# Kernel optimization log

Measured on AMD Instinct MI355X. Metric: run time of the kernel, lower is better.

Reference implementation:

```python
import jax, jax.numpy as jnp
import numpy as np

EPS = 1e-6


def _make_coord_3d(D, H, W, dtype):
    # torch make_coord_3d(flatten=False).permute(3,0,1,2): channels stacked as (x, y, z)
    lz = jnp.linspace(-1.0, 1.0, D, dtype=dtype)
    ly = jnp.linspace(-1.0, 1.0, H, dtype=dtype)
    lx = jnp.linspace(-1.0, 1.0, W, dtype=dtype)
    cz, cy, cx = jnp.meshgrid(lz, ly, lx, indexing='ij')
    return jnp.stack([cx, cy, cz], axis=0)  # [3, D, H, W]


def _trilinear_border(vol, gd, gh, gw):
    # vol: [C, D, H, W]; gd/gh/gw: [Q] normalized coords for the D/H/W axes.
    # Matches torch grid_sample(mode='bilinear', align_corners=False, padding_mode='border').
    C, D, H, W = vol.shape
    z = (gd + 1.0) * (D * 0.5) - 0.5
    y = (gh + 1.0) * (H * 0.5) - 0.5
    x = (gw + 1.0) * (W * 0.5) - 0.5
    z0 = jnp.floor(z); y0 = jnp.floor(y); x0 = jnp.floor(x)
    wz = (z - z0)[None]; wy = (y - y0)[None]; wx = (x - x0)[None]  # [1, Q]
    z0i = jnp.clip(z0.astype(jnp.int32), 0, D - 1); z1i = jnp.clip(z0.astype(jnp.int32) + 1, 0, D - 1)
    y0i = jnp.clip(y0.astype(jnp.int32), 0, H - 1); y1i = jnp.clip(y0.astype(jnp.int32) + 1, 0, H - 1)
    x0i = jnp.clip(x0.astype(jnp.int32), 0, W - 1); x1i = jnp.clip(x0.astype(jnp.int32) + 1, 0, W - 1)
    g = lambda zi, yi, xi: vol[:, zi, yi, xi]  # gather -> [C, Q]
    return (g(z0i, y0i, x0i) * (1 - wz) * (1 - wy) * (1 - wx)
            + g(z0i, y0i, x1i) * (1 - wz) * (1 - wy) * wx
            + g(z0i, y1i, x0i) * (1 - wz) * wy * (1 - wx)
            + g(z0i, y1i, x1i) * (1 - wz) * wy * wx
            + g(z1i, y0i, x0i) * wz * (1 - wy) * (1 - wx)
            + g(z1i, y0i, x1i) * wz * (1 - wy) * wx
            + g(z1i, y1i, x0i) * wz * wy * (1 - wx)
            + g(z1i, y1i, x1i) * wz * wy * wx)


def _forward(inp, coord, cell, W0, b0, W1, b1, W2, b2, W3, b3):
    feat = inp  # identity encoder: inp is the latent feature grid
    B, C, D, H, W = feat.shape
    rx = 2.0 / D / 2.0; ry = 2.0 / H / 2.0; rz = 2.0 / W / 2.0
    sizes = jnp.array([D, H, W], dtype=feat.dtype)
    feat_coord = _make_coord_3d(D, H, W, feat.dtype)  # [3, D, H, W]
    sample_b = jax.vmap(_trilinear_border, in_axes=(0, 0, 0, 0))
    sample_c = jax.vmap(_trilinear_border, in_axes=(None, 0, 0, 0))

    rel_cell = cell * sizes  # [B, Q, 3]
    cell_vol = jnp.abs(cell[..., 0] * cell[..., 1] * cell[..., 2])
    scale_sq = jnp.clip(8.0 / (cell_vol + 1e-8), 1.0, 64.0)[..., None]  # [B, Q, 1]

    def mlp(x):
        h = jax.nn.relu(x @ W0 + b0)
        h = jax.nn.relu(h @ W1 + b1)
        h = jax.nn.relu(h @ W2 + b2)
        return h @ W3 + b3

    preds, areas = [], []
    for vx in (-1, 1):
        for vy in (-1, 1):
            for vz in (-1, 1):
                shift = jnp.array([vx * rx + EPS, vy * ry + EPS, vz * rz + EPS], dtype=coord.dtype)
                c = jnp.clip(coord + shift, -1.0 + 1e-6, 1.0 - 1e-6)
                gd, gh, gw = c[..., 0], c[..., 1], c[..., 2]
                q_feat = sample_b(feat, gd, gh, gw).transpose(0, 2, 1)        # [B, Q, C]
                q_coord = sample_c(feat_coord, gd, gh, gw).transpose(0, 2, 1)  # [B, Q, 3]
                rel_coord = (coord - q_coord) * sizes
                x = jnp.concatenate([q_feat, rel_coord, rel_cell, scale_sq], axis=-1)
                preds.append(mlp(x))  # [B, Q, 1]
                areas.append(jnp.abs(rel_coord[..., 0] * rel_coord[..., 1] * rel_coord[..., 2]) + 1e-9)
    tot_area = jnp.stack(areas).sum(axis=0)
    areas = areas[::-1]  # local-ensemble diagonal-swap of areas
    ret = sum(p * (a / tot_area)[..., None] for p, a in zip(preds, areas))
    return ret


def setup_inputs() -> dict:
    key = jax.random.key(0)
    ks = jax.random.split(key, 8)
    B, C, D, Q, HID = 1, 64, 32, 131072, 256
    in_dim = C + 3 + 3 + 1  # 71
    w = lambda k, shape, fan_in: jax.random.normal(k, shape, jnp.float32) * (1.0 / np.sqrt(fan_in))
    inp = jax.random.normal(ks[0], (B, C, D, D, D), jnp.float32)
    coord = jax.random.uniform(ks[1], (B, Q, 3), jnp.float32, -1.0, 1.0)
    cell = jnp.full((B, Q, 3), 2.0 / 64.0, jnp.float32)  # uniform cell size of a 64^3 query grid
    return {
        'inp': inp, 'coord': coord, 'cell': cell,
        'W0': w(ks[2], (in_dim, HID), in_dim), 'b0': jnp.zeros((HID,), jnp.float32),
        'W1': w(ks[3], (HID, HID), HID), 'b1': jnp.zeros((HID,), jnp.float32),
        'W2': w(ks[4], (HID, HID), HID), 'b2': jnp.zeros((HID,), jnp.float32),
        'W3': w(ks[5], (HID, 1), HID), 'b3': jnp.zeros((1,), jnp.float32),
    }


def reference(inp, coord, cell, W0, b0, W1, b1, W2, b2, W3, b3):
    return _forward(inp, coord, cell, W0, b0, W1, b1, W2, b2, W3, b3)
```

## Files before the change

kernel.cpp:

```cpp
#include <hip/hip_runtime.h>

typedef __attribute__((ext_vector_type(8))) short s16x8;
typedef __attribute__((ext_vector_type(4))) float f32x4;

__device__ __forceinline__ unsigned short f2bf(float x) {
  unsigned u = __float_as_uint(x);
  u = (u + 0x7fffu + ((u >> 16) & 1u)) >> 16;
  return (unsigned short)u;
}
__device__ __forceinline__ unsigned cvt_pk_bf16(float a, float b) {
  unsigned r;
  asm("v_cvt_pk_bf16_f32 %0, %1, %2" : "=v"(r) : "v"(a), "v"(b));
  return r;
}
__device__ __forceinline__ float bflo(unsigned v) { return __uint_as_float(v << 16); }
__device__ __forceinline__ float bfhi(unsigned v) { return __uint_as_float(v & 0xffff0000u); }

__device__ __forceinline__ void lgkm_barrier() {
  asm volatile("s_waitcnt lgkmcnt(0)" ::: "memory");
  __builtin_amdgcn_s_barrier();
  asm volatile("" ::: "memory");
}

#define FEAT_OFF 0
#define W0F_OFF  2097152
#define W1F_OFF  (W0F_OFF + 24576)
#define W2F_OFF  (W1F_OFF + 65536)
#define W3P_OFF  (W2F_OFF + 65536)
#define WS_TOTAL (W3P_OFF + 512)

__device__ __forceinline__ int col_log(int kp) {
  return (kp & 0xC0) | ((kp & 3) << 4) | ((kp >> 2) & 15);
}

__global__ void liif_prep(const float* __restrict__ inp,
                          const float* __restrict__ W0,
                          const float* __restrict__ W1,
                          const float* __restrict__ W2,
                          const float* __restrict__ W3,
                          unsigned short* __restrict__ ws) {
  int tid = blockIdx.x * 256 + threadIdx.x;
  if (tid < 2097152) {
    int pos = tid >> 6, c = tid & 63;
    ws[FEAT_OFF + tid] = f2bf(inp[c * 32768 + pos]);
  } else if (tid < W1F_OFF) {
    int e = tid - W0F_OFF;
    int j = e & 7, L = (e >> 3) & 63, nt = (e >> 9) & 15, c = e >> 13;
    int k = c * 32 + (L >> 4) * 8 + j, n = nt * 16 + (L & 15);
    ws[tid] = (k < 71) ? f2bf(W0[k * 256 + n]) : (unsigned short)0;
  } else if (tid < W2F_OFF) {
    int e = tid - W1F_OFF;
    int j = e & 7, L = (e >> 3) & 63, nt = (e >> 9) & 15, c = e >> 13;
    int kp = c * 32 + (L >> 4) * 8 + j, n = nt * 16 + (L & 15);
    ws[tid] = f2bf(W1[col_log(kp) * 256 + n]);
  } else if (tid < W3P_OFF) {
    int e = tid - W2F_OFF;
    int j = e & 7, L = (e >> 3) & 63, nt = (e >> 9) & 15, c = e >> 13;
    int kp = c * 32 + (L >> 4) * 8 + j, n = nt * 16 + (L & 15);
    ws[tid] = f2bf(W2[col_log(kp) * 256 + n]);
  } else if (tid < W3P_OFF + 256) {
    int e = tid - W3P_OFF;
    float* w3p = (float*)(ws + W3P_OFF);
    w3p[e] = W3[col_log(e)];
  }
}

template<int KC, bool PRE>
__device__ __forceinline__ void run_layer(const unsigned short* __restrict__ Wf,
                                          const float* __restrict__ bias,
                                          const unsigned short* A, int astride,
                                          unsigned short* H,
                                          const unsigned short* __restrict__ Wnext,
                                          s16x8 (&nb)[4],
                                          int wave, int quad, int l16, int lane) {
  f32x4 acc[4][4];
#pragma unroll
  for (int ntl = 0; ntl < 4; ++ntl) {
    float bv = bias[(wave * 4 + ntl) * 16 + l16];
    f32x4 ai = (f32x4){bv, bv, bv, bv};
#pragma unroll
    for (int rt = 0; rt < 4; ++rt) acc[rt][ntl] = ai;
  }

  __builtin_amdgcn_s_setprio(1);
#pragma unroll
  for (int c = 0; c < KC; ++c) {
    s16x8 a[4];
#pragma unroll
    for (int rt = 0; rt < 4; ++rt)
      a[rt] = *(const s16x8*)(A + (rt * 16 + l16) * astride + c * 32 + quad * 8);
#pragma unroll
    for (int ntl = 0; ntl < 4; ++ntl) {
      int nt = wave * 4 + ntl;
      s16x8 b = (c == 0) ? nb[ntl]
                         : *(const s16x8*)(Wf + (((c * 16 + nt) * 64 + lane) << 3));
#pragma unroll
      for (int rt = 0; rt < 4; ++rt)
        acc[rt][ntl] = __builtin_amdgcn_mfma_f32_16x16x32_bf16(a[rt], b, acc[rt][ntl], 0, 0, 0);
    }
  }
  __builtin_amdgcn_s_setprio(0);

  if constexpr (PRE) {
#pragma unroll
    for (int ntl = 0; ntl < 4; ++ntl)
      nb[ntl] = *(const s16x8*)(Wnext + (((wave * 4 + ntl) * 64 + lane) << 3));
  }

  lgkm_barrier();

  const int cbase = wave * 64 + l16 * 4;
#pragma unroll
  for (int rt = 0; rt < 4; ++rt) {
#pragma unroll
    for (int i = 0; i < 4; ++i) {
      float v0 = fmaxf(acc[rt][0][i], 0.0f);
      float v1 = fmaxf(acc[rt][1][i], 0.0f);
      float v2 = fmaxf(acc[rt][2][i], 0.0f);
      float v3 = fmaxf(acc[rt][3][i], 0.0f);
      int r = rt * 16 + quad * 4 + i;
      uint2 pw = make_uint2(cvt_pk_bf16(v0, v1), cvt_pk_bf16(v2, v3));
      *(uint2*)(H + r * 264 + cbase) = pw;
    }
  }
  lgkm_barrier();
}

__global__ __launch_bounds__(256, 4)
void liif_main(const float* __restrict__ coord,
               const float* __restrict__ cell,
               const float* __restrict__ b0,
               const float* __restrict__ b1,
               const float* __restrict__ b2,
               const float* __restrict__ b3,
               const unsigned short* __restrict__ ws,
               float* __restrict__ out) {
  __shared__ __align__(16) unsigned short sm_h[64 * 264];
  __shared__ float sm_area[64];
  __shared__ float sm_pred[64];
  unsigned short* sm_x = sm_h;

  const unsigned short* feat = ws + FEAT_OFF;
  const int tid = threadIdx.x;
  const int lane = tid & 63;
  const int wave = tid >> 6;
  const int quad = lane >> 4;
  const int l16 = lane & 15;

  s16x8 nb[4];
#pragma unroll
  for (int ntl = 0; ntl < 4; ++ntl)
    nb[ntl] = *(const s16x8*)(ws + W0F_OFF + (((wave * 4 + ntl) * 64 + lane) << 3));

  {
    const int row = tid >> 2, p = tid & 3;
    const int ql = row >> 3, s = row & 7;
    const int q = blockIdx.x * 8 + ql;
    const float c0r = coord[q * 3 + 0], c1r = coord[q * 3 + 1], c2r = coord[q * 3 + 2];
    const float R = 0.03125f;
    const float sh0 = ((s & 4) ? R : -R) + 1e-6f;
    const float sh1 = ((s & 2) ? R : -R) + 1e-6f;
    const float sh2 = ((s & 1) ? R : -R) + 1e-6f;
    const float LO = -1.0f + 1e-6f, HI = 1.0f - 1e-6f;
    float c0 = fminf(fmaxf(c0r + sh0, LO), HI);
    float c1 = fminf(fmaxf(c1r + sh1, LO), HI);
    float c2 = fminf(fmaxf(c2r + sh2, LO), HI);
    float z = (c0 + 1.0f) * 16.0f - 0.5f;
    float y = (c1 + 1.0f) * 16.0f - 0.5f;
    float x = (c2 + 1.0f) * 16.0f - 0.5f;
    float zf = floorf(z), yf = floorf(y), xf = floorf(x);
    float wz = z - zf, wy = y - yf, wx = x - xf;
    int z0 = min(max((int)zf, 0), 31), z1 = min(max((int)zf + 1, 0), 31);
    int y0 = min(max((int)yf, 0), 31), y1 = min(max((int)yf + 1, 0), 31);
    int x0 = min(max((int)xf, 0), 31), x1 = min(max((int)xf + 1, 0), 31);
    float wz0 = 1.0f - wz, wy0 = 1.0f - wy, wx0 = 1.0f - wx;

    float w[8] = { wz0 * wy0 * wx0, wz0 * wy0 * wx, wz0 * wy * wx0, wz0 * wy * wx,
                   wz  * wy0 * wx0, wz  * wy0 * wx, wz  * wy * wx0, wz  * wy * wx };
    int idx[8] = { (z0 * 32 + y0) * 32 + x0, (z0 * 32 + y0) * 32 + x1,
                   (z0 * 32 + y1) * 32 + x0, (z0 * 32 + y1) * 32 + x1,
                   (z1 * 32 + y0) * 32 + x0, (z1 * 32 + y0) * 32 + x1,
                   (z1 * 32 + y1) * 32 + x0, (z1 * 32 + y1) * 32 + x1 };

    float acc[16];
#pragma unroll
    for (int i = 0; i < 16; ++i) acc[i] = 0.0f;
#pragma unroll
    for (int corner = 0; corner < 8; ++corner) {
      const uint4* cp = (const uint4*)(feat + idx[corner] * 64 + p * 16);
      uint4 v0 = cp[0], v1 = cp[1];
      float wc = w[corner];
      unsigned vv[8] = { v0.x, v0.y, v0.z, v0.w, v1.x, v1.y, v1.z, v1.w };
#pragma unroll
      for (int d = 0; d < 8; ++d) {
        acc[2 * d]     += wc * bflo(vv[d]);
        acc[2 * d + 1] += wc * bfhi(vv[d]);
      }
    }
    unsigned pw[8];
#pragma unroll
    for (int d = 0; d < 8; ++d)
      pw[d] = cvt_pk_bf16(acc[2 * d], acc[2 * d + 1]);
    uint4* dst = (uint4*)(&sm_x[row * 104 + p * 16]);
    dst[0] = make_uint4(pw[0], pw[1], pw[2], pw[3]);
    dst[1] = make_uint4(pw[4], pw[5], pw[6], pw[7]);

    if (p == 0) {
      const float step = 2.0f / 31.0f;
      float qc0 = wx0 * (-1.0f + step * x0) + wx * (-1.0f + step * x1);
      float qc1 = wy0 * (-1.0f + step * y0) + wy * (-1.0f + step * y1);
      float qc2 = wz0 * (-1.0f + step * z0) + wz * (-1.0f + step * z1);
      float rel0 = (c0r - qc0) * 32.0f;
      float rel1 = (c1r - qc1) * 32.0f;
      float rel2 = (c2r - qc2) * 32.0f;
      sm_area[row] = fabsf(rel0 * rel1 * rel2) + 1e-9f;
      float cl0 = cell[q * 3 + 0], cl1 = cell[q * 3 + 1], cl2 = cell[q * 3 + 2];
      float ssq = fminf(fmaxf(8.0f / (fabsf(cl0 * cl1 * cl2) + 1e-8f), 1.0f), 64.0f);
      unsigned tw0 = cvt_pk_bf16(rel0, rel1);
      unsigned tw1 = cvt_pk_bf16(rel2, cl0 * 32.0f);
      unsigned tw2 = cvt_pk_bf16(cl1 * 32.0f, cl2 * 32.0f);
      unsigned tw3 = cvt_pk_bf16(ssq, 0.0f);
      uint4* d2 = (uint4*)(&sm_x[row * 104 + 64]);
      d2[0] = make_uint4(tw0, tw1, tw2, tw3);
      d2[1] = make_uint4(0, 0, 0, 0);
      d2[2] = make_uint4(0, 0, 0, 0);
      d2[3] = make_uint4(0, 0, 0, 0);
    }
  }
  lgkm_barrier();

  run_layer<3, true >(ws + W0F_OFF, b0, sm_x, 104, sm_h, ws + W1F_OFF, nb, wave, quad, l16, lane);
  run_layer<8, true >(ws + W1F_OFF, b1, sm_h, 264, sm_h, ws + W2F_OFF, nb, wave, quad, l16, lane);
  run_layer<8, false>(ws + W2F_OFF, b2, sm_h, 264, sm_h, nullptr,      nb, wave, quad, l16, lane);

  {
    const int row = tid >> 2, p = tid & 3;
    const unsigned short* hp = sm_h + row * 264 + p * 64;
    const float* W3p = (const float*)(ws + W3P_OFF);
    float sum = 0.0f;
#pragma unroll
    for (int kk = 0; kk < 8; ++kk) {
      const uint4 v = *(const uint4*)(hp + kk * 8);
      const float4 wa = *(const float4*)(W3p + p * 64 + kk * 8);
      const float4 wb = *(const float4*)(W3p + p * 64 + kk * 8 + 4);
      sum += wa.x * bflo(v.x) + wa.y * bfhi(v.x);
      sum += wa.z * bflo(v.y) + wa.w * bfhi(v.y);
      sum += wb.x * bflo(v.z) + wb.y * bfhi(v.z);
      sum += wb.z * bflo(v.w) + wb.w * bfhi(v.w);
    }
    sum += __shfl_xor(sum, 1);
    sum += __shfl_xor(sum, 2);
    if (p == 0) sm_pred[row] = sum + b3[0];
  }
  lgkm_barrier();

  if (tid < 8) {
    const int ql = tid;
    float tot = 0.0f, ret = 0.0f;
#pragma unroll
    for (int s = 0; s < 8; ++s) tot += sm_area[ql * 8 + s];
#pragma unroll
    for (int s = 0; s < 8; ++s) ret += sm_pred[ql * 8 + s] * sm_area[ql * 8 + (7 - s)];
    out[blockIdx.x * 8 + ql] = ret / tot;
  }
}

extern "C" void kernel_launch(void* const* d_in, const int* in_sizes, int n_in,
                              void* d_out, int out_size, void* d_ws, size_t ws_size,
                              hipStream_t stream) {
  const float* inp   = (const float*)d_in[0];
  const float* coord = (const float*)d_in[1];
  const float* cell  = (const float*)d_in[2];
  const float* W0    = (const float*)d_in[3];
  const float* b0    = (const float*)d_in[4];
  const float* W1    = (const float*)d_in[5];
  const float* b1    = (const float*)d_in[6];
  const float* W2    = (const float*)d_in[7];
  const float* b2    = (const float*)d_in[8];
  const float* W3    = (const float*)d_in[9];
  const float* b3    = (const float*)d_in[10];
  unsigned short* ws = (unsigned short*)d_ws;
  float* out = (float*)d_out;

  const int Q = in_sizes[1] / 3;
  hipLaunchKernelGGL(liif_prep, dim3((WS_TOTAL + 255) / 256), dim3(256), 0, stream,
                     inp, W0, W1, W2, W3, ws);
  hipLaunchKernelGGL(liif_main, dim3(Q / 8), dim3(256), 0, stream,
                     coord, cell, b0, b1, b2, b3, ws, out);
}
```

Measured before the change: 435.4 us.

## Ping-pong two half-block tiles to overlap sampling, MLP layers and epilogue

Doubles the block to 512 threads that handle two 64-row tiles, offset by one stage, so one half samples or runs the scalar final layer while the other half runs MFMA layers. It also replaces the padded LDS row stride with an XOR swizzle to avoid bank conflicts, and does the final area-weighted combine with shuffles instead of shared arrays. The cost is more barriers per block, two 32KB LDS buffers, and launch bounds that no longer force four blocks per CU, so occupancy and register pressure may change.

New measurement: 633.1 us. 1.45x slower.

```diff
diff --git a/kernel.cpp b/kernel.cpp
--- a/kernel.cpp
+++ b/kernel.cpp
@@ -31,6 +31,9 @@
 
 __device__ __forceinline__ int col_log(int kp) {
   return (kp & 0xC0) | ((kp & 3) << 4) | ((kp >> 2) & 15);
+}
+__device__ __forceinline__ int hswz(int row, int col) {
+  return row * 256 + (col ^ ((row & 7) << 3));
 }
 
 __global__ void liif_prep(const float* __restrict__ inp,
@@ -65,51 +68,51 @@
   }
 }
 
-template<int KC, bool PRE>
-__device__ __forceinline__ void run_layer(const unsigned short* __restrict__ Wf,
-                                          const float* __restrict__ bias,
-                                          const unsigned short* A, int astride,
-                                          unsigned short* H,
-                                          const unsigned short* __restrict__ Wnext,
-                                          s16x8 (&nb)[4],
-                                          int wave, int quad, int l16, int lane) {
-  f32x4 acc[4][4];
+template<int KC, bool PRE, bool SWZ>
+__device__ __forceinline__ void layer_mfma(f32x4 (&acc)[4][4],
+                                           const unsigned short* __restrict__ Wf,
+                                           const float* __restrict__ bias,
+                                           const unsigned short* A,
+                                           const unsigned short* __restrict__ Wnext,
+                                           s16x8 (&nb)[4],
+                                           int wave4, int quad, int l16, int lane) {
 #pragma unroll
   for (int ntl = 0; ntl < 4; ++ntl) {
-    float bv = bias[(wave * 4 + ntl) * 16 + l16];
+    float bv = bias[(wave4 * 4 + ntl) * 16 + l16];
     f32x4 ai = (f32x4){bv, bv, bv, bv};
 #pragma unroll
     for (int rt = 0; rt < 4; ++rt) acc[rt][ntl] = ai;
   }
-
   __builtin_amdgcn_s_setprio(1);
 #pragma unroll
   for (int c = 0; c < KC; ++c) {
     s16x8 a[4];
 #pragma unroll
-    for (int rt = 0; rt < 4; ++rt)
-      a[rt] = *(const s16x8*)(A + (rt * 16 + l16) * astride + c * 32 + quad * 8);
+    for (int rt = 0; rt < 4; ++rt) {
+      int row = rt * 16 + l16, col = c * 32 + quad * 8;
+      int idx = SWZ ? hswz(row, col) : row * 104 + col;
+      a[rt] = *(const s16x8*)(A + idx);
+    }
 #pragma unroll
     for (int ntl = 0; ntl < 4; ++ntl) {
-      int nt = wave * 4 + ntl;
       s16x8 b = (c == 0) ? nb[ntl]
-                         : *(const s16x8*)(Wf + (((c * 16 + nt) * 64 + lane) << 3));
+                         : *(const s16x8*)(Wf + (((c * 16 + wave4 * 4 + ntl) * 64 + lane) << 3));
 #pragma unroll
       for (int rt = 0; rt < 4; ++rt)
         acc[rt][ntl] = __builtin_amdgcn_mfma_f32_16x16x32_bf16(a[rt], b, acc[rt][ntl], 0, 0, 0);
     }
   }
   __builtin_amdgcn_s_setprio(0);
-
   if constexpr (PRE) {
 #pragma unroll
     for (int ntl = 0; ntl < 4; ++ntl)
-      nb[ntl] = *(const s16x8*)(Wnext + (((wave * 4 + ntl) * 64 + lane) << 3));
-  }
-
-  lgkm_barrier();
-
-  const int cbase = wave * 64 + l16 * 4;
+      nb[ntl] = *(const s16x8*)(Wnext + (((wave4 * 4 + ntl) * 64 + lane) << 3));
+  }
+}
+
+__device__ __forceinline__ void layer_epi(f32x4 (&acc)[4][4], unsigned short* H,
+                                          int wave4, int quad, int l16) {
+  const int cb = wave4 * 64 + l16 * 4;
 #pragma unroll
   for (int rt = 0; rt < 4; ++rt) {
 #pragma unroll
@@ -120,13 +123,129 @@
       float v3 = fmaxf(acc[rt][3][i], 0.0f);
       int r = rt * 16 + quad * 4 + i;
       uint2 pw = make_uint2(cvt_pk_bf16(v0, v1), cvt_pk_bf16(v2, v3));
-      *(uint2*)(H + r * 264 + cbase) = pw;
+      *(uint2*)(H + hswz(r, cb)) = pw;
     }
   }
-  lgkm_barrier();
-}
-
-__global__ __launch_bounds__(256, 4)
+}
+
+__device__ __forceinline__ void sample_tile(const unsigned short* __restrict__ feat,
+                                            const float* __restrict__ coord,
+                                            const float* __restrict__ cell,
+                                            unsigned short* T, int qbase,
+                                            int htid, float& area) {
+  const int row = htid >> 2, p = htid & 3;
+  const int ql = row >> 3, s = row & 7;
+  const int q = qbase + ql;
+  const float c0r = coord[q * 3 + 0], c1r = coord[q * 3 + 1], c2r = coord[q * 3 + 2];
+  const float R = 0.03125f;
+  const float sh0 = ((s & 4) ? R : -R) + 1e-6f;
+  const float sh1 = ((s & 2) ? R : -R) + 1e-6f;
+  const float sh2 = ((s & 1) ? R : -R) + 1e-6f;
+  const float LO = -1.0f + 1e-6f, HI = 1.0f - 1e-6f;
+  float c0 = fminf(fmaxf(c0r + sh0, LO), HI);
+  float c1 = fminf(fmaxf(c1r + sh1, LO), HI);
+  float c2 = fminf(fmaxf(c2r + sh2, LO), HI);
+  float z = (c0 + 1.0f) * 16.0f - 0.5f;
+  float y = (c1 + 1.0f) * 16.0f - 0.5f;
+  float x = (c2 + 1.0f) * 16.0f - 0.5f;
+  float zf = floorf(z), yf = floorf(y), xf = floorf(x);
+  float wz = z - zf, wy = y - yf, wx = x - xf;
+  int z0 = min(max((int)zf, 0), 31), z1 = min(max((int)zf + 1, 0), 31);
+  int y0 = min(max((int)yf, 0), 31), y1 = min(max((int)yf + 1, 0), 31);
+  int x0 = min(max((int)xf, 0), 31), x1 = min(max((int)xf + 1, 0), 31);
+  float wz0 = 1.0f - wz, wy0 = 1.0f - wy, wx0 = 1.0f - wx;
+
+  float w[8] = { wz0 * wy0 * wx0, wz0 * wy0 * wx, wz0 * wy * wx0, wz0 * wy * wx,
+                 wz  * wy0 * wx0, wz  * wy0 * wx, wz  * wy * wx0, wz  * wy * wx };
+  int idx[8] = { (z0 * 32 + y0) * 32 + x0, (z0 * 32 + y0) * 32 + x1,
+                 (z0 * 32 + y1) * 32 + x0, (z0 * 32 + y1) * 32 + x1,
+                 (z1 * 32 + y0) * 32 + x0, (z1 * 32 + y0) * 32 + x1,
+                 (z1 * 32 + y1) * 32 + x0, (z1 * 32 + y1) * 32 + x1 };
+
+  float acc[16];
+#pragma unroll
+  for (int i = 0; i < 16; ++i) acc[i] = 0.0f;
+#pragma unroll
+  for (int corner = 0; corner < 8; ++corner) {
+    const uint4* cp = (const uint4*)(feat + idx[corner] * 64 + p * 16);
+    uint4 v0 = cp[0], v1 = cp[1];
+    float wc = w[corner];
+    unsigned vv[8] = { v0.x, v0.y, v0.z, v0.w, v1.x, v1.y, v1.z, v1.w };
+#pragma unroll
+    for (int d = 0; d < 8; ++d) {
+      acc[2 * d]     += wc * bflo(vv[d]);
+      acc[2 * d + 1] += wc * bfhi(vv[d]);
+    }
+  }
+  unsigned pw[8];
+#pragma unroll
+  for (int d = 0; d < 8; ++d)
+    pw[d] = cvt_pk_bf16(acc[2 * d], acc[2 * d + 1]);
+  uint4* dst = (uint4*)(T + row * 104 + p * 16);
+  dst[0] = make_uint4(pw[0], pw[1], pw[2], pw[3]);
+  dst[1] = make_uint4(pw[4], pw[5], pw[6], pw[7]);
+
+  if (p == 0) {
+    const float step = 2.0f / 31.0f;
+    float qc0 = wx0 * (-1.0f + step * x0) + wx * (-1.0f + step * x1);
+    float qc1 = wy0 * (-1.0f + step * y0) + wy * (-1.0f + step * y1);
+    float qc2 = wz0 * (-1.0f + step * z0) + wz * (-1.0f + step * z1);
+    float rel0 = (c0r - qc0) * 32.0f;
+    float rel1 = (c1r - qc1) * 32.0f;
+    float rel2 = (c2r - qc2) * 32.0f;
+    area = fabsf(rel0 * rel1 * rel2) + 1e-9f;
+    float cl0 = cell[q * 3 + 0], cl1 = cell[q * 3 + 1], cl2 = cell[q * 3 + 2];
+    float ssq = fminf(fmaxf(8.0f / (fabsf(cl0 * cl1 * cl2) + 1e-8f), 1.0f), 64.0f);
+    unsigned tw0 = cvt_pk_bf16(rel0, rel1);
+    unsigned tw1 = cvt_pk_bf16(rel2, cl0 * 32.0f);
+    unsigned tw2 = cvt_pk_bf16(cl1 * 32.0f, cl2 * 32.0f);
+    unsigned tw3 = cvt_pk_bf16(ssq, 0.0f);
+    uint4* d2 = (uint4*)(T + row * 104 + 64);
+    d2[0] = make_uint4(tw0, tw1, tw2, tw3);
+    d2[1] = make_uint4(0, 0, 0, 0);
+    d2[2] = make_uint4(0, 0, 0, 0);
+    d2[3] = make_uint4(0, 0, 0, 0);
+  }
+}
+
+__device__ __forceinline__ void l3_combine(const unsigned short* T,
+                                           const float* __restrict__ W3p,
+                                           const float* __restrict__ b3,
+                                           float area, float* __restrict__ out,
+                                           int qbase, int htid, int lane) {
+  const int row = htid >> 2, p = htid & 3;
+  float sum = 0.0f;
+#pragma unroll
+  for (int kk = 0; kk < 8; ++kk) {
+    int col = p * 64 + kk * 8;
+    const uint4 v = *(const uint4*)(T + hswz(row, col));
+    const float4 wa = *(const float4*)(W3p + col);
+    const float4 wb = *(const float4*)(W3p + col + 4);
+    sum += wa.x * bflo(v.x) + wa.y * bfhi(v.x);
+    sum += wa.z * bflo(v.y) + wa.w * bfhi(v.y);
+    sum += wb.x * bflo(v.z) + wb.y * bfhi(v.z);
+    sum += wb.z * bflo(v.w) + wb.w * bfhi(v.w);
+  }
+  sum += __shfl_xor(sum, 1);
+  sum += __shfl_xor(sum, 2);
+  float pred = sum + b3[0];
+  const int base = lane & 32;
+  float tot = 0.0f, ret = 0.0f;
+#pragma unroll
+  for (int s = 0; s < 8; ++s) {
+    float as = __shfl(area, base + 4 * s, 64);
+    float ar = __shfl(area, base + 4 * (7 - s), 64);
+    float ps = __shfl(pred, base + 4 * s, 64);
+    tot += as;
+    ret += ps * ar;
+  }
+  if ((lane & 31) == 0) {
+    int ql = ((htid >> 6) << 1) + (lane >> 5);
+    out[qbase + ql] = ret / tot;
+  }
+}
+
+__global__ __launch_bounds__(512)
 void liif_main(const float* __restrict__ coord,
                const float* __restrict__ cell,
                const float* __restrict__ b0,
@@ -135,134 +254,62 @@
                const float* __restrict__ b3,
                const unsigned short* __restrict__ ws,
                float* __restrict__ out) {
-  __shared__ __align__(16) unsigned short sm_h[64 * 264];
-  __shared__ float sm_area[64];
-  __shared__ float sm_pred[64];
-  unsigned short* sm_x = sm_h;
+  __shared__ __align__(16) unsigned short smA[64 * 256];
+  __shared__ __align__(16) unsigned short smB[64 * 256];
 
   const unsigned short* feat = ws + FEAT_OFF;
+  const float* W3p = (const float*)(ws + W3P_OFF);
   const int tid = threadIdx.x;
   const int lane = tid & 63;
   const int wave = tid >> 6;
+  const int half = wave >> 2;
+  const int wave4 = wave & 3;
   const int quad = lane >> 4;
   const int l16 = lane & 15;
+  const int htid = tid & 255;
+  unsigned short* myT = half ? smB : smA;
+  const int qb = blockIdx.x * 16;
 
   s16x8 nb[4];
 #pragma unroll
   for (int ntl = 0; ntl < 4; ++ntl)
-    nb[ntl] = *(const s16x8*)(ws + W0F_OFF + (((wave * 4 + ntl) * 64 + lane) << 3));
-
-  {
-    const int row = tid >> 2, p = tid & 3;
-    const int ql = row >> 3, s = row & 7;
-    const int q = blockIdx.x * 8 + ql;
-    const float c0r = coord[q * 3 + 0], c1r = coord[q * 3 + 1], c2r = coord[q * 3 + 2];
-    const float R = 0.03125f;
-    const float sh0 = ((s & 4) ? R : -R) + 1e-6f;
-    const float sh1 = ((s & 2) ? R : -R) + 1e-6f;
-    const float sh2 = ((s & 1) ? R : -R) + 1e-6f;
-    const float LO = -1.0f + 1e-6f, HI = 1.0f - 1e-6f;
-    float c0 = fminf(fmaxf(c0r + sh0, LO), HI);
-    float c1 = fminf(fmaxf(c1r + sh1, LO), HI);
-    float c2 = fminf(fmaxf(c2r + sh2, LO), HI);
-    float z = (c0 + 1.0f) * 16.0f - 0.5f;
-    float y = (c1 + 1.0f) * 16.0f - 0.5f;
-    float x = (c2 + 1.0f) * 16.0f - 0.5f;
-    float zf = floorf(z), yf = floorf(y), xf = floorf(x);
-    float wz = z - zf, wy = y - yf, wx = x - xf;
-    int z0 = min(max((int)zf, 0), 31), z1 = min(max((int)zf + 1, 0), 31);
-    int y0 = min(max((int)yf, 0), 31), y1 = min(max((int)yf + 1, 0), 31);
-    int x0 = min(max((int)xf, 0), 31), x1 = min(max((int)xf + 1, 0), 31);
-    float wz0 = 1.0f - wz, wy0 = 1.0f - wy, wx0 = 1.0f - wx;
-
-    float w[8] = { wz0 * wy0 * wx0, wz0 * wy0 * wx, wz0 * wy * wx0, wz0 * wy * wx,
-                   wz  * wy0 * wx0, wz  * wy0 * wx, wz  * wy * wx0, wz  * wy * wx };
-    int idx[8] = { (z0 * 32 + y0) * 32 + x0, (z0 * 32 + y0) * 32 + x1,
-                   (z0 * 32 + y1) * 32 + x0, (z0 * 32 + y1) * 32 + x1,
-                   (z1 * 32 + y0) * 32 + x0, (z1 * 32 + y0) * 32 + x1,
-                   (z1 * 32 + y1) * 32 + x0, (z1 * 32 + y1) * 32 + x1 };
-
-    float acc[16];
-#pragma unroll
-    for (int i = 0; i < 16; ++i) acc[i] = 0.0f;
-#pragma unroll
-    for (int corner = 0; corner < 8; ++corner) {
-      const uint4* cp = (const uint4*)(feat + idx[corner] * 64 + p * 16);
-      uint4 v0 = cp[0], v1 = cp[1];
-      float wc = w[corner];
-      unsigned vv[8] = { v0.x, v0.y, v0.z, v0.w, v1.x, v1.y, v1.z, v1.w };
-#pragma unroll
-      for (int d = 0; d < 8; ++d) {
-        acc[2 * d]     += wc * bflo(vv[d]);
-        acc[2 * d + 1] += wc * bfhi(vv[d]);
-      }
-    }
-    unsigned pw[8];
-#pragma unroll
-    for (int d = 0; d < 8; ++d)
-      pw[d] = cvt_pk_bf16(acc[2 * d], acc[2 * d + 1]);
-    uint4* dst = (uint4*)(&sm_x[row * 104 + p * 16]);
-    dst[0] = make_uint4(pw[0], pw[1], pw[2], pw[3]);
-    dst[1] = make_uint4(pw[4], pw[5], pw[6], pw[7]);
-
-    if (p == 0) {
-      const float step = 2.0f / 31.0f;
-      float qc0 = wx0 * (-1.0f + step * x0) + wx * (-1.0f + step * x1);
-      float qc1 = wy0 * (-1.0f + step * y0) + wy * (-1.0f + step * y1);
-      float qc2 = wz0 * (-1.0f + step * z0) + wz * (-1.0f + step * z1);
-      float rel0 = (c0r - qc0) * 32.0f;
-      float rel1 = (c1r - qc1) * 32.0f;
-      float rel2 = (c2r - qc2) * 32.0f;
-      sm_area[row] = fabsf(rel0 * rel1 * rel2) + 1e-9f;
-      float cl0 = cell[q * 3 + 0], cl1 = cell[q * 3 + 1], cl2 = cell[q * 3 + 2];
-      float ssq = fminf(fmaxf(8.0f / (fabsf(cl0 * cl1 * cl2) + 1e-8f), 1.0f), 64.0f);
-      unsigned tw0 = cvt_pk_bf16(rel0, rel1);
-      unsigned tw1 = cvt_pk_bf16(rel2, cl0 * 32.0f);
-      unsigned tw2 = cvt_pk_bf16(cl1 * 32.0f, cl2 * 32.0f);
-      unsigned tw3 = cvt_pk_bf16(ssq, 0.0f);
-      uint4* d2 = (uint4*)(&sm_x[row * 104 + 64]);
-      d2[0] = make_uint4(tw0, tw1, tw2, tw3);
-      d2[1] = make_uint4(0, 0, 0, 0);
-      d2[2] = make_uint4(0, 0, 0, 0);
-      d2[3] = make_uint4(0, 0, 0, 0);
-    }
-  }
-  lgkm_barrier();
-
-  run_layer<3, true >(ws + W0F_OFF, b0, sm_x, 104, sm_h, ws + W1F_OFF, nb, wave, quad, l16, lane);
-  run_layer<8, true >(ws + W1F_OFF, b1, sm_h, 264, sm_h, ws + W2F_OFF, nb, wave, quad, l16, lane);
-  run_layer<8, false>(ws + W2F_OFF, b2, sm_h, 264, sm_h, nullptr,      nb, wave, quad, l16, lane);
-
-  {
-    const int row = tid >> 2, p = tid & 3;
-    const unsigned short* hp = sm_h + row * 264 + p * 64;
-    const float* W3p = (const float*)(ws + W3P_OFF);
-    float sum = 0.0f;
-#pragma unroll
-    for (int kk = 0; kk < 8; ++kk) {
-      const uint4 v = *(const uint4*)(hp + kk * 8);
-      const float4 wa = *(const float4*)(W3p + p * 64 + kk * 8);
-      const float4 wb = *(const float4*)(W3p + p * 64 + kk * 8 + 4);
-      sum += wa.x * bflo(v.x) + wa.y * bfhi(v.x);
-      sum += wa.z * bflo(v.y) + wa.w * bfhi(v.y);
-      sum += wb.x * bflo(v.z) + wb.y * bfhi(v.z);
-      sum += wb.z * bflo(v.w) + wb.w * bfhi(v.w);
-    }
-    sum += __shfl_xor(sum, 1);
-    sum += __shfl_xor(sum, 2);
-    if (p == 0) sm_pred[row] = sum + b3[0];
-  }
-  lgkm_barrier();
-
-  if (tid < 8) {
-    const int ql = tid;
-    float tot = 0.0f, ret = 0.0f;
-#pragma unroll
-    for (int s = 0; s < 8; ++s) tot += sm_area[ql * 8 + s];
-#pragma unroll
-    for (int s = 0; s < 8; ++s) ret += sm_pred[ql * 8 + s] * sm_area[ql * 8 + (7 - s)];
-    out[blockIdx.x * 8 + ql] = ret / tot;
-  }
+    nb[ntl] = *(const s16x8*)(ws + W0F_OFF + (((wave4 * 4 + ntl) * 64 + lane) << 3));
+
+  float area = 0.0f;
+  f32x4 acc[4][4];
+
+  if (half == 0) sample_tile(feat, coord, cell, smA, qb, htid, area);
+  lgkm_barrier();
+  if (half == 0)
+    layer_mfma<3, true, false>(acc, ws + W0F_OFF, b0, smA, ws + W1F_OFF, nb, wave4, quad, l16, lane);
+  else
+    sample_tile(feat, coord, cell, smB, qb + 8, htid, area);
+  lgkm_barrier();
+  if (half == 0) layer_epi(acc, smA, wave4, quad, l16);
+  lgkm_barrier();
+  if (half == 0)
+    layer_mfma<8, true, true>(acc, ws + W1F_OFF, b1, smA, ws + W2F_OFF, nb, wave4, quad, l16, lane);
+  else
+    layer_mfma<3, true, false>(acc, ws + W0F_OFF, b0, smB, ws + W1F_OFF, nb, wave4, quad, l16, lane);
+  lgkm_barrier();
+  layer_epi(acc, myT, wave4, quad, l16);
+  lgkm_barrier();
+  if (half == 0)
+    layer_mfma<8, false, true>(acc, ws + W2F_OFF, b2, smA, nullptr, nb, wave4, quad, l16, lane);
+  else
+    layer_mfma<8, true, true>(acc, ws + W1F_OFF, b1, smB, ws + W2F_OFF, nb, wave4, quad, l16, lane);
+  lgkm_barrier();
+  layer_epi(acc, myT, wave4, quad, l16);
+  lgkm_barrier();
+  if (half == 0)
+    l3_combine(smA, W3p, b3, area, out, qb, htid, lane);
+  else
+    layer_mfma<8, false, true>(acc, ws + W2F_OFF, b2, smB, nullptr, nb, wave4, quad, l16, lane);
+  lgkm_barrier();
+  if (half == 1) layer_epi(acc, smB, wave4, quad, l16);
+  lgkm_barrier();
+  if (half == 1)
+    l3_combine(smB, W3p, b3, area, out, qb + 8, htid, lane);
 }
 
 extern "C" void kernel_launch(void* const* d_in, const int* in_sizes, int n_in,
@@ -285,6 +332,6 @@
   const int Q = in_sizes[1] / 3;
   hipLaunchKernelGGL(liif_prep, dim3((WS_TOTAL + 255) / 256), dim3(256), 0, stream,
                      inp, W0, W1, W2, W3, ws);
-  hipLaunchKernelGGL(liif_main, dim3(Q / 8), dim3(256), 0, stream,
+  hipLaunchKernelGGL(liif_main, dim3(Q / 16), dim3(512), 0, stream,
                      coord, cell, b0, b1, b2, b3, ws, out);
 }
```

## Swizzle hidden-activation LDS layout and shrink LDS to raise occupancy

Applied to the files above, without the earlier changes.

Replaces the padded 264-stride hidden buffer with a compact 256-stride layout that uses an XOR swizzle to avoid LDS bank conflicts, and removes the area and pred shared arrays. The final area-weighted ensemble now uses wave shuffles instead of a barrier plus shared memory. Launch bounds go from 4 to 5 blocks per SM, and the trilinear accumulation is written with packed float2 math. The goal is more resident blocks and fewer barriers, at the cost of tighter register limits and extra index arithmetic.

After: 1.142 ms. +162.3%, slower.

```diff
diff --git a/kernel.cpp b/kernel.cpp
--- a/kernel.cpp
+++ b/kernel.cpp
@@ -2,6 +2,7 @@
 
 typedef __attribute__((ext_vector_type(8))) short s16x8;
 typedef __attribute__((ext_vector_type(4))) float f32x4;
+typedef __attribute__((ext_vector_type(2))) float f32x2;
 
 __device__ __forceinline__ unsigned short f2bf(float x) {
   unsigned u = __float_as_uint(x);
@@ -31,6 +32,9 @@
 
 __device__ __forceinline__ int col_log(int kp) {
   return (kp & 0xC0) | ((kp & 3) << 4) | ((kp >> 2) & 15);
+}
+__device__ __forceinline__ int hswz(int row, int col) {
+  return row * 256 + (col ^ ((row & 7) << 3));
 }
 
 __global__ void liif_prep(const float* __restrict__ inp,
@@ -65,10 +69,10 @@
   }
 }
 
-template<int KC, bool PRE>
+template<int KC, bool PRE, bool SWZ>
 __device__ __forceinline__ void run_layer(const unsigned short* __restrict__ Wf,
                                           const float* __restrict__ bias,
-                                          const unsigned short* A, int astride,
+                                          const unsigned short* A,
                                           unsigned short* H,
                                           const unsigned short* __restrict__ Wnext,
                                           s16x8 (&nb)[4],
@@ -87,8 +91,11 @@
   for (int c = 0; c < KC; ++c) {
     s16x8 a[4];
 #pragma unroll
-    for (int rt = 0; rt < 4; ++rt)
-      a[rt] = *(const s16x8*)(A + (rt * 16 + l16) * astride + c * 32 + quad * 8);
+    for (int rt = 0; rt < 4; ++rt) {
+      int row = rt * 16 + l16, col = c * 32 + quad * 8;
+      int idx = SWZ ? hswz(row, col) : row * 104 + col;
+      a[rt] = *(const s16x8*)(A + idx);
+    }
 #pragma unroll
     for (int ntl = 0; ntl < 4; ++ntl) {
       int nt = wave * 4 + ntl;
@@ -109,7 +116,7 @@
 
   lgkm_barrier();
 
-  const int cbase = wave * 64 + l16 * 4;
+  const int cb = wave * 64 + l16 * 4;
 #pragma unroll
   for (int rt = 0; rt < 4; ++rt) {
 #pragma unroll
@@ -120,13 +127,13 @@
       float v3 = fmaxf(acc[rt][3][i], 0.0f);
       int r = rt * 16 + quad * 4 + i;
       uint2 pw = make_uint2(cvt_pk_bf16(v0, v1), cvt_pk_bf16(v2, v3));
-      *(uint2*)(H + r * 264 + cbase) = pw;
+      *(uint2*)(H + hswz(r, cb)) = pw;
     }
   }
   lgkm_barrier();
 }
 
-__global__ __launch_bounds__(256, 4)
+__global__ __launch_bounds__(256, 5)
 void liif_main(const float* __restrict__ coord,
                const float* __restrict__ cell,
                const float* __restrict__ b0,
@@ -135,27 +142,29 @@
                const float* __restrict__ b3,
                const unsigned short* __restrict__ ws,
                float* __restrict__ out) {
-  __shared__ __align__(16) unsigned short sm_h[64 * 264];
-  __shared__ float sm_area[64];
-  __shared__ float sm_pred[64];
+  __shared__ __align__(16) unsigned short sm_h[64 * 256];
   unsigned short* sm_x = sm_h;
 
   const unsigned short* feat = ws + FEAT_OFF;
+  const float* W3p = (const float*)(ws + W3P_OFF);
   const int tid = threadIdx.x;
   const int lane = tid & 63;
   const int wave = tid >> 6;
   const int quad = lane >> 4;
   const int l16 = lane & 15;
+  const int qb = blockIdx.x * 8;
 
   s16x8 nb[4];
 #pragma unroll
   for (int ntl = 0; ntl < 4; ++ntl)
     nb[ntl] = *(const s16x8*)(ws + W0F_OFF + (((wave * 4 + ntl) * 64 + lane) << 3));
+
+  float area = 0.0f;
 
   {
     const int row = tid >> 2, p = tid & 3;
     const int ql = row >> 3, s = row & 7;
-    const int q = blockIdx.x * 8 + ql;
+    const int q = qb + ql;
     const float c0r = coord[q * 3 + 0], c1r = coord[q * 3 + 1], c2r = coord[q * 3 + 2];
     const float R = 0.03125f;
     const float sh0 = ((s & 4) ? R : -R) + 1e-6f;
@@ -182,25 +191,26 @@
                    (z1 * 32 + y0) * 32 + x0, (z1 * 32 + y0) * 32 + x1,
                    (z1 * 32 + y1) * 32 + x0, (z1 * 32 + y1) * 32 + x1 };
 
-    float acc[16];
-#pragma unroll
-    for (int i = 0; i < 16; ++i) acc[i] = 0.0f;
+    f32x2 acc2[8];
+#pragma unroll
+    for (int i = 0; i < 8; ++i) acc2[i] = (f32x2){0.f, 0.f};
 #pragma unroll
     for (int corner = 0; corner < 8; ++corner) {
       const uint4* cp = (const uint4*)(feat + idx[corner] * 64 + p * 16);
       uint4 v0 = cp[0], v1 = cp[1];
       float wc = w[corner];
+      f32x2 wc2 = (f32x2){wc, wc};
       unsigned vv[8] = { v0.x, v0.y, v0.z, v0.w, v1.x, v1.y, v1.z, v1.w };
 #pragma unroll
       for (int d = 0; d < 8; ++d) {
-        acc[2 * d]     += wc * bflo(vv[d]);
-        acc[2 * d + 1] += wc * bfhi(vv[d]);
+        f32x2 xv = (f32x2){bflo(vv[d]), bfhi(vv[d])};
+        acc2[d] += wc2 * xv;
       }
     }
     unsigned pw[8];
 #pragma unroll
     for (int d = 0; d < 8; ++d)
-      pw[d] = cvt_pk_bf16(acc[2 * d], acc[2 * d + 1]);
+      pw[d] = cvt_pk_bf16(acc2[d].x, acc2[d].y);
     uint4* dst = (uint4*)(&sm_x[row * 104 + p * 16]);
     dst[0] = make_uint4(pw[0], pw[1], pw[2], pw[3]);
     dst[1] = make_uint4(pw[4], pw[5], pw[6], pw[7]);
@@ -213,7 +223,7 @@
       float rel0 = (c0r - qc0) * 32.0f;
       float rel1 = (c1r - qc1) * 32.0f;
       float rel2 = (c2r - qc2) * 32.0f;
-      sm_area[row] = fabsf(rel0 * rel1 * rel2) + 1e-9f;
+      area = fabsf(rel0 * rel1 * rel2) + 1e-9f;
       float cl0 = cell[q * 3 + 0], cl1 = cell[q * 3 + 1], cl2 = cell[q * 3 + 2];
       float ssq = fminf(fmaxf(8.0f / (fabsf(cl0 * cl1 * cl2) + 1e-8f), 1.0f), 64.0f);
       unsigned tw0 = cvt_pk_bf16(rel0, rel1);
@@ -229,20 +239,19 @@
   }
   lgkm_barrier();
 
-  run_layer<3, true >(ws + W0F_OFF, b0, sm_x, 104, sm_h, ws + W1F_OFF, nb, wave, quad, l16, lane);
-  run_layer<8, true >(ws + W1F_OFF, b1, sm_h, 264, sm_h, ws + W2F_OFF, nb, wave, quad, l16, lane);
-  run_layer<8, false>(ws + W2F_OFF, b2, sm_h, 264, sm_h, nullptr,      nb, wave, quad, l16, lane);
+  run_layer<3, true,  false>(ws + W0F_OFF, b0, sm_x, sm_h, ws + W1F_OFF, nb, wave, quad, l16, lane);
+  run_layer<8, true,  true >(ws + W1F_OFF, b1, sm_h, sm_h, ws + W2F_OFF, nb, wave, quad, l16, lane);
+  run_layer<8, false, true >(ws + W2F_OFF, b2, sm_h, sm_h, nullptr,      nb, wave, quad, l16, lane);
 
   {
     const int row = tid >> 2, p = tid & 3;
-    const unsigned short* hp = sm_h + row * 264 + p * 64;
-    const float* W3p = (const float*)(ws + W3P_OFF);
     float sum = 0.0f;
 #pragma unroll
     for (int kk = 0; kk < 8; ++kk) {
-      const uint4 v = *(const uint4*)(hp + kk * 8);
-      const float4 wa = *(const float4*)(W3p + p * 64 + kk * 8);
-      const float4 wb = *(const float4*)(W3p + p * 64 + kk * 8 + 4);
+      int col = p * 64 + kk * 8;
+      const uint4 v = *(const uint4*)(sm_h + hswz(row, col));
+      const float4 wa = *(const float4*)(W3p + col);
+      const float4 wb = *(const float4*)(W3p + col + 4);
       sum += wa.x * bflo(v.x) + wa.y * bfhi(v.x);
       sum += wa.z * bflo(v.y) + wa.w * bfhi(v.y);
       sum += wb.x * bflo(v.z) + wb.y * bfhi(v.z);
@@ -250,18 +259,21 @@
     }
     sum += __shfl_xor(sum, 1);
     sum += __shfl_xor(sum, 2);
-    if (p == 0) sm_pred[row] = sum + b3[0];
-  }
-  lgkm_barrier();
-
-  if (tid < 8) {
-    const int ql = tid;
+    float pred = sum + b3[0];
+    const int base = lane & 32;
     float tot = 0.0f, ret = 0.0f;
 #pragma unroll
-    for (int s = 0; s < 8; ++s) tot += sm_area[ql * 8 + s];
-#pragma unroll
-    for (int s = 0; s < 8; ++s) ret += sm_pred[ql * 8 + s] * sm_area[ql * 8 + (7 - s)];
-    out[blockIdx.x * 8 + ql] = ret / tot;
+    for (int s = 0; s < 8; ++s) {
+      float as = __shfl(area, base + 4 * s, 64);
+      float ar = __shfl(area, base + 4 * (7 - s), 64);
+      float ps = __shfl(pred, base + 4 * s, 64);
+      tot += as;
+      ret += ps * ar;
+    }
+    if ((lane & 31) == 0) {
+      int ql = (wave << 1) + (lane >> 5);
+      out[qb + ql] = ret / tot;
+    }
   }
 }
 
```
